# Performance work log

Hardware: AMD Instinct MI355X
Metric: run time of the kernel (lower is better)

The kernel has to match this reference:

```python
import jax, jax.numpy as jnp
import numpy as np
import math

DIM = 512      # vMF embedding dim
B = 512        # batch
K = 10         # sample_size
C = 8192       # num_classes
L = 0.7        # kappa_confidence
T_REJ = 32     # fixed rejection-sampling tries (acceptance ~0.7 per try)


def _vmf_logc(k, dim=DIM):
    # Approximate log normalizer from the paper (approximate_logc=True path).
    nm14 = (dim - 1) / 4.0
    nm12 = (dim - 1) / 2.0
    np12 = (dim + 1) / 2.0
    sqrtm = jnp.sqrt(nm12 * nm12 + k * k)
    sqrtp = jnp.sqrt(np12 * np12 + k * k)
    return nm14 * (jnp.log(nm12 + sqrtm) + jnp.log(nm12 + sqrtp)) - 0.5 * (sqrtm + sqrtp)


def _split(params):
    # params layout: [log_probs(1), means(DIM), hidden_ik(1)] (single component).
    means = params[..., 1:1 + DIM]
    hidden_ik = params[..., -1]
    mu = means / jnp.linalg.norm(means, axis=-1, keepdims=True)
    kappa = 1.0 / jnp.exp(hidden_ik)  # positive(x) = exp(x) parametrization
    return mu, kappa


def _vmf_sample(key, mu, kappa, n):
    # Wood's algorithm, vectorized over (b, n) with fixed-count rejection.
    b, d = mu.shape
    kap = kappa[:, None]  # (b,1)
    bb = (-2.0 * kap + jnp.sqrt(4.0 * kap * kap + (d - 1) ** 2)) / (d - 1)
    x0 = (1.0 - bb) / (1.0 + bb)
    cc = kap * x0 + (d - 1) * jnp.log(1.0 - x0 * x0)
    kz, ku, kv = jax.random.split(key, 3)
    z = jax.random.beta(kz, (d - 1) / 2.0, (d - 1) / 2.0, (T_REJ, b, n))
    w = (1.0 - (1.0 + bb) * z) / (1.0 - (1.0 - bb) * z)  # (T,b,n)
    u = jax.random.uniform(ku, (T_REJ, b, n), minval=1e-10)
    acc = kap * w + (d - 1) * jnp.log(1.0 - x0 * w) - cc >= jnp.log(u)
    idx = jnp.argmax(acc, axis=0)  # first accepted try
    w_sel = jnp.take_along_axis(w, idx[None], axis=0)[0]  # (b,n)
    v = jax.random.normal(kv, (b, n, d))
    v = v - jnp.einsum('bnd,bd->bn', v, mu)[..., None] * mu[:, None, :]
    v = v / jnp.linalg.norm(v, axis=-1, keepdims=True)
    sin_t = jnp.sqrt(jnp.clip(1.0 - w_sel * w_sel, 0.0))
    return w_sel[..., None] * mu[:, None, :] + sin_t[..., None] * v  # (b,n,d)


def setup_inputs() -> dict:
    key = jax.random.key(0)
    kp, kw, kl = jax.random.split(key, 3)
    # Input distribution parameters: random means, hidden_ik ~ log(1/kappa) with realistic kappa.
    parameters = jax.random.normal(kp, (B, DIM + 2), dtype=jnp.float32)
    kappa0 = L / (1.0 - L * L) * (DIM - 1) / math.sqrt(DIM)  # ~31
    parameters = parameters.at[:, -1].set(0.1 * parameters[:, -1] - math.log(kappa0))
    # Class weight, built exactly as in __init__ (non-deterministic target).
    means = jax.random.normal(kw, (C, DIM), dtype=jnp.float32) * (L / (1.0 - L * L) * (DIM - 1) / math.sqrt(DIM))
    norm = jnp.linalg.norm(means, axis=-1, keepdims=True)
    hidden_ik = jnp.log(1.0 / norm)  # ipositive = log
    weight = jnp.concatenate([jnp.zeros((C, 1), jnp.float32), means, hidden_ik], axis=-1)
    log_scale = jnp.asarray(2.773, dtype=jnp.float32)
    labels = jax.random.randint(kl, (B,), 0, C)
    return {"parameters": parameters, "weight": weight, "log_scale": log_scale, "labels": labels}


def reference(parameters, weight, log_scale, labels):
    scale = jnp.exp(log_scale)
    mu_x, kappa_x = _split(parameters)   # (b,d), (b,)
    mu_w, kappa_w = _split(weight)       # (c,d), (c,)
    sample = _vmf_sample(jax.random.key(42), mu_x, kappa_x, K)  # (b,K,d)
    sample = sample / jnp.linalg.norm(sample, axis=-1, keepdims=True)
    # logmls(b,k,c): samples have concentration k1=scale; since all means are unit,
    # ||k1*m1 + k2*m2|| = sqrt(k1^2 + k2^2 + 2*k1*k2*cos) -> single GEMM over d.
    cos = jnp.einsum('bkd,cd->bkc', sample, mu_w)
    k1 = scale
    k2 = kappa_w
    kk = jnp.sqrt(k1 * k1 + k2 * k2 + 2.0 * k1 * (k2 * cos))  # (b,K,c)
    logmls = _vmf_logc(k1) + _vmf_logc(k2)[None, None, :] - _vmf_logc(kk)
    neg_logden = jax.scipy.special.logsumexp(logmls, axis=2) - _vmf_logc(scale)  # (b,K)
    neg_lognum = scale * jnp.einsum('bd,bd->b', mu_x, mu_w[labels])
    losses = neg_logden.mean(axis=1) - neg_lognum  # (b,)
    b = parameters.shape[0]
    logits = jnp.zeros((b, C), parameters.dtype).at[jnp.arange(b), labels].set(-losses)
    return logits
```

## Files before the change

kernel.cpp:

```cpp
#include <hip/hip_runtime.h>
#include <stdint.h>

#define DIMD 512
#define BATCH 512
#define KSAMP 10
#define NCLS 8192
#define TREJ 32

typedef float f32x4 __attribute__((ext_vector_type(4)));
typedef long l2 __attribute__((ext_vector_type(2)));

__device__ inline uint64_t sm64(uint64_t x) {
  x += 0x9E3779B97F4A7C15ull;
  x = (x ^ (x >> 30)) * 0xBF58476D1CE4E5B9ull;
  x = (x ^ (x >> 27)) * 0x94D049BB133111EBull;
  return x ^ (x >> 31);
}
__device__ inline float u01(uint32_t u) {
  return ((float)u + 0.5f) * 2.3283064365386963e-10f;
}
__device__ inline float normal_from(uint64_t r) {
  float u1 = u01((uint32_t)(r >> 32));
  float u2 = u01((uint32_t)r);
  return sqrtf(-2.0f * __logf(u1)) * __cosf(6.28318530718f * u2);
}
__device__ inline float gamma255(uint64_t& ctr) {
  const float dg = 255.1666667f;
  const float cg = 0.02086730f;
  for (int i = 0; i < 16; i++) {
    uint64_t r = sm64(ctr++);
    float x = normal_from(r);
    float t = fmaf(cg, x, 1.0f);
    if (t <= 0.0f) continue;
    float v3 = t * t * t;
    uint64_t r2 = sm64(ctr++);
    float u3 = u01((uint32_t)(r2 >> 32));
    if (__logf(u3) < 0.5f * x * x + dg * (1.0f - v3 + __logf(v3))) return dg * v3;
  }
  return dg;
}
__device__ inline float wave_sum(float v) {
  #pragma unroll
  for (int o = 32; o > 0; o >>= 1) v += __shfl_down(v, o, 64);
  return __shfl(v, 0, 64);
}
__device__ inline float vmf_logc(float k) {
  float k2 = k * k;
  float sm = sqrtf(65280.25f + k2);
  float sp = sqrtf(65792.25f + k2);
  return 127.75f * (__logf(255.5f + sm) + __logf(255.5f + sp)) - 0.5f * (sm + sp);
}
__device__ inline int2 pack_fp8x8(const float* v, float s) {
  int lo = 0, hi = 0;
  lo = __builtin_amdgcn_cvt_pk_fp8_f32(v[0] * s, v[1] * s, lo, false);
  lo = __builtin_amdgcn_cvt_pk_fp8_f32(v[2] * s, v[3] * s, lo, true);
  hi = __builtin_amdgcn_cvt_pk_fp8_f32(v[4] * s, v[5] * s, hi, false);
  hi = __builtin_amdgcn_cvt_pk_fp8_f32(v[6] * s, v[7] * s, hi, true);
  return make_int2(lo, hi);
}
__device__ inline int pk_off(int l) {
  return ((l >> 3) << 6) + ((l & 3) << 4) + (((l & 7) < 4) ? 0 : 8);
}
__device__ inline void sync_lds() {
  asm volatile("s_waitcnt lgkmcnt(0)\n\ts_barrier" ::: "memory");
}

__global__ __launch_bounds__(256) void prep_sample(const float* __restrict__ weight,
                                                   const float* __restrict__ params,
                                                   const float* __restrict__ lscale,
                                                   unsigned char* __restrict__ muW8,
                                                   float4* __restrict__ cparams,
                                                   float* __restrict__ rowsum,
                                                   float4* __restrict__ out4,
                                                   unsigned char* __restrict__ Sb8) {
  int blk = blockIdx.x, tid = threadIdx.x;
  int wave = tid >> 6, lane = tid & 63;
  if (blk < 2048) {
    out4[(size_t)blk * 512 + tid]       = make_float4(0.f, 0.f, 0.f, 0.f);
    out4[(size_t)blk * 512 + 256 + tid] = make_float4(0.f, 0.f, 0.f, 0.f);
    if (blk < 20) rowsum[blk * 256 + tid] = 0.0f;

    int c = blk * 4 + wave;
    const float* wr = weight + (size_t)c * (DIMD + 2) + 1;
    float v[8];
    float n2 = 0.0f;
    #pragma unroll
    for (int j = 0; j < 8; j++) { v[j] = wr[lane * 8 + j]; n2 += v[j] * v[j]; }
    n2 = wave_sum(n2);
    float inv = rsqrtf(n2) * 16.0f;
    int2 pk = pack_fp8x8(v, inv);
    *(int2*)(muW8 + (size_t)c * 512 + pk_off(lane)) = pk;

    float hik = wr[DIMD];
    float kw = __expf(-hik);
    float k1 = __expf(lscale[0]);
    float lcw = vmf_logc(kw);
    float A2 = fmaf(k1, k1, kw * kw);
    float B2 = 2.0f * k1 * kw;
    const float X0 = 0.9238795f, X1 = 0.3826834f;
    int l3 = lane & 3;
    float Xj = (l3 == 0) ? X0 : (l3 == 1) ? X1 : (l3 == 2) ? -X1 : -X0;
    float gj = lcw - vmf_logc(sqrtf(fmaf(B2, Xj, A2)));
    float g0 = __shfl(gj, 0, 64), g1 = __shfl(gj, 1, 64);
    float g2 = __shfl(gj, 2, 64), g3 = __shfl(gj, 3, 64);
    if (lane == 0) {
      float b0 = 0.25f * (g0 + g1 + g2 + g3);
      float b1 = 0.5f * (X0 * (g0 - g3) + X1 * (g1 - g2));
      float b2 = 0.5f * 0.7071068f * ((g0 + g3) - (g1 + g2));
      float b3 = 0.5f * (X1 * (g0 - g3) - X0 * (g1 - g2));
      const float L2E = 1.4426950409f;
      const float S1 = 1.0f / 256.0f;
      cparams[c] = make_float4((b0 - b2) * L2E, (b1 - 3.0f * b3) * L2E * S1,
                               (2.0f * b2) * L2E * S1 * S1,
                               (4.0f * b3) * L2E * S1 * S1 * S1);
    }
  } else {
    int row = (blk - 2048) * 4 + wave;
    int b = row / KSAMP;
    const float* pr = params + (size_t)b * (DIMD + 2) + 1;

    float mu[8];
    float n2 = 0.0f;
    #pragma unroll
    for (int j = 0; j < 8; j++) { mu[j] = pr[lane * 8 + j]; n2 += mu[j] * mu[j]; }
    n2 = wave_sum(n2);
    float invn = rsqrtf(n2);
    #pragma unroll
    for (int j = 0; j < 8; j++) mu[j] *= invn;

    float kap = __expf(-pr[DIMD]);
    float bb = (-2.0f * kap + sqrtf(fmaf(4.0f * kap, kap, 511.0f * 511.0f))) / 511.0f;
    float x0 = (1.0f - bb) / (1.0f + bb);
    float cc = kap * x0 + 511.0f * __logf(1.0f - x0 * x0);

    uint64_t ctr = (((uint64_t)(row + 1)) << 32) | ((uint64_t)lane << 8);
    float g1 = gamma255(ctr);
    float g2 = gamma255(ctr);
    float z = g1 / (g1 + g2);
    float wt = (1.0f - (1.0f + bb) * z) / (1.0f - (1.0f - bb) * z);
    uint64_t r = sm64(ctr++);
    float u = u01((uint32_t)(r >> 32));
    float lhs = kap * wt + 511.0f * __logf(1.0f - x0 * wt) - cc;
    bool acc = (lane < TREJ) && (lhs >= __logf(fmaxf(u, 1e-10f)));
    uint64_t mask = __ballot(acc);
    int sel = mask ? (__ffsll((unsigned long long)mask) - 1) : 0;
    float w = __shfl(wt, sel, 64);

    uint64_t cbase = (((uint64_t)(row + 1)) << 32) | 0x40000000ull;
    float v[8];
    #pragma unroll
    for (int j = 0; j < 8; j++) v[j] = normal_from(sm64(cbase + (uint64_t)(lane * 8 + j)));
    float d = 0.0f;
    #pragma unroll
    for (int j = 0; j < 8; j++) d += v[j] * mu[j];
    d = wave_sum(d);
    float t2 = 0.0f;
    #pragma unroll
    for (int j = 0; j < 8; j++) { v[j] -= d * mu[j]; t2 += v[j] * v[j]; }
    t2 = wave_sum(t2);
    float ivt = rsqrtf(t2);
    float st = sqrtf(fmaxf(0.0f, 1.0f - w * w)) * ivt;
    float sv[8];
    float s2 = 0.0f;
    #pragma unroll
    for (int j = 0; j < 8; j++) { sv[j] = fmaf(st, v[j], w * mu[j]); s2 += sv[j] * sv[j]; }
    s2 = wave_sum(s2);
    float is = rsqrtf(s2) * 16.0f;
    int2 pk = pack_fp8x8(sv, is);
    *(int2*)(Sb8 + (size_t)row * 512 + pk_off(lane)) = pk;
  }
}

__global__ __launch_bounds__(512, 4) void gemm_lse(const unsigned char* __restrict__ Sb8,
                                                   const unsigned char* __restrict__ Wb8,
                                                   const float4* __restrict__ cparams,
                                                   float* __restrict__ rowsum) {
  __shared__ __align__(16) unsigned char As[2][256 * 64];
  __shared__ __align__(16) unsigned char Bs[2][128 * 64];
  int tid = threadIdx.x;
  int lane = tid & 63, wave = tid >> 6;
  int tx = lane & 15, tz = lane >> 4;

  int id = blockIdx.x;
  int xcd = id & 7, lid = id >> 3;
  int c0 = (xcd * 8 + (lid & 7)) * 128;
  int r0 = (lid >> 3) * 256;

  int srow = lane >> 2;
  int slot = lane & 3;
  int kg = slot ^ ((srow >> 1) & 3);
  const unsigned char* gA[2];
  const unsigned char* gB;
  #pragma unroll
  for (int c = 0; c < 2; c++)
    gA[c] = Sb8 + (size_t)(r0 + (wave * 2 + c) * 16 + srow) * 512 + kg * 16;
  gB = Wb8 + (size_t)(c0 + wave * 16 + srow) * 512 + kg * 16;
  int ldsAo = (wave * 2) * 1024 + lane * 16;
  int ldsBo = wave * 1024 + lane * 16;

  int wm = wave >> 1, wn = wave & 1;

  f32x4 acc[4][4];
  #pragma unroll
  for (int i = 0; i < 4; i++)
    #pragma unroll
    for (int j = 0; j < 4; j++) acc[i][j] = (f32x4){0.f, 0.f, 0.f, 0.f};

  int4 ar0[2], br0[1];
  int4 ar1[2], br1[1];

#define LOADCH(CI, AR, BR)                                   \
  { AR[0] = *(const int4*)(gA[0] + (CI) * 64);               \
    AR[1] = *(const int4*)(gA[1] + (CI) * 64);               \
    BR[0] = *(const int4*)(gB + (CI) * 64); }

#define WRITELDS(P, AR, BR)                                  \
  { *(int4*)&As[P][ldsAo]        = AR[0];                    \
    *(int4*)&As[P][ldsAo + 1024] = AR[1];                    \
    *(int4*)&Bs[P][ldsBo]        = BR[0]; }

#define COMPUTE(P)                                                        \
  { l2 af[4]; l2 bf[4];                                                   \
    int sA_ = tz ^ ((tx >> 1) & 3);                                       \
    _Pragma("unroll")                                                     \
    for (int mi = 0; mi < 4; mi++)                                        \
      af[mi] = *(const l2*)&As[P][(wm * 64 + mi * 16 + tx) * 64 + sA_ * 16]; \
    _Pragma("unroll")                                                     \
    for (int ni = 0; ni < 4; ni++)                                        \
      bf[ni] = *(const l2*)&Bs[P][(wn * 64 + ni * 16 + tx) * 64 + sA_ * 16]; \
    __builtin_amdgcn_s_setprio(1);                                        \
    _Pragma("unroll")                                                     \
    for (int mi = 0; mi < 4; mi++)                                        \
      _Pragma("unroll")                                                   \
      for (int ni = 0; ni < 4; ni++)                                      \
        acc[mi][ni] = __builtin_amdgcn_mfma_f32_16x16x32_fp8_fp8(af[mi].x, bf[ni].x, acc[mi][ni], 0, 0, 0); \
    _Pragma("unroll")                                                     \
    for (int mi = 0; mi < 4; mi++)                                        \
      _Pragma("unroll")                                                   \
      for (int ni = 0; ni < 4; ni++)                                      \
        acc[mi][ni] = __builtin_amdgcn_mfma_f32_16x16x32_fp8_fp8(af[mi].y, bf[ni].y, acc[mi][ni], 0, 0, 0); \
    __builtin_amdgcn_s_setprio(0);                                        \
  }

  LOADCH(0, ar0, br0);
  LOADCH(1, ar1, br1);
  WRITELDS(0, ar0, br0);
  sync_lds();

#define GITER_EVEN(IT)                                       \
  { if ((IT) + 2 < 8) LOADCH((IT) + 2, ar0, br0);            \
    COMPUTE(0);                                              \
    if ((IT) + 1 < 8) WRITELDS(1, ar1, br1);                 \
    if ((IT) < 7) sync_lds(); }

#define GITER_ODD(IT)                                        \
  { if ((IT) + 2 < 8) LOADCH((IT) + 2, ar1, br1);            \
    COMPUTE(1);                                              \
    if ((IT) + 1 < 8) WRITELDS(0, ar0, br0);                 \
    if ((IT) < 7) sync_lds(); }

  GITER_EVEN(0) GITER_ODD(1) GITER_EVEN(2) GITER_ODD(3)
  GITER_EVEN(4) GITER_ODD(5) GITER_EVEN(6) GITER_ODD(7)

  float4 cp[4];
  #pragma unroll
  for (int ni = 0; ni < 4; ni++) cp[ni] = cparams[c0 + wn * 64 + ni * 16 + tx];

  #pragma unroll
  for (int mi = 0; mi < 4; mi++) {
    #pragma unroll
    for (int reg = 0; reg < 4; reg++) {
      float s = 0.0f;
      #pragma unroll
      for (int ni = 0; ni < 4; ni++) {
        float cv = acc[mi][ni][reg];
        float g = fmaf(fmaf(fmaf(cp[ni].w, cv, cp[ni].z), cv, cp[ni].y), cv, cp[ni].x);
        s += exp2f(g);
      }
      #pragma unroll
      for (int o = 1; o < 16; o <<= 1) s += __shfl_xor(s, o, 64);
      if (tx == 0)
        atomicAdd(&rowsum[r0 + wm * 64 + mi * 16 + tz * 4 + reg], s);
    }
  }
}

__global__ __launch_bounds__(64) void finalize_kernel(const float* __restrict__ params,
                                                      const float* __restrict__ weight,
                                                      const float* __restrict__ rowsum,
                                                      const int* __restrict__ labels,
                                                      const float* __restrict__ lscale,
                                                      float* __restrict__ out) {
  int b = blockIdx.x;
  int lane = threadIdx.x;
  int lab = labels[b];
  const float* pr = params + (size_t)b * (DIMD + 2) + 1;
  const float* wr = weight + (size_t)lab * (DIMD + 2) + 1;
  float nx = 0.0f, nw = 0.0f, d = 0.0f;
  #pragma unroll
  for (int j = 0; j < 8; j++) {
    float xv = pr[j * 64 + lane];
    float wv = wr[j * 64 + lane];
    nx += xv * xv; nw += wv * wv; d += xv * wv;
  }
  nx = wave_sum(nx); nw = wave_sum(nw); d = wave_sum(d);
  if (lane == 0) {
    float k1 = expf(lscale[0]);
    float acc = 0.0f;
    #pragma unroll
    for (int k = 0; k < KSAMP; k++) acc += __logf(rowsum[b * KSAMP + k]);
    float loss = acc * (1.0f / KSAMP) - k1 * d * rsqrtf(nx) * rsqrtf(nw);
    out[(size_t)b * NCLS + lab] = -loss;
  }
}

extern "C" void kernel_launch(void* const* d_in, const int* in_sizes, int n_in,
                              void* d_out, int out_size, void* d_ws, size_t ws_size,
                              hipStream_t stream) {
  const float* params = (const float*)d_in[0];
  const float* weight = (const float*)d_in[1];
  const float* lscale = (const float*)d_in[2];
  const int*   labels = (const int*)d_in[3];
  float* out = (float*)d_out;
  char* ws = (char*)d_ws;

  unsigned char* muW8    = (unsigned char*)(ws);
  unsigned char* Sb8     = (unsigned char*)(ws + 4194304);
  float4*        cparams = (float4*)(ws + 6815744);
  float*         rowsum  = (float*)(ws + 6946816);

  hipLaunchKernelGGL(prep_sample, dim3(2048 + BATCH * KSAMP / 4), dim3(256), 0, stream,
                     weight, params, lscale, muW8, cparams, rowsum, (float4*)out, Sb8);
  hipLaunchKernelGGL(gemm_lse, dim3((NCLS / 128) * (BATCH * KSAMP / 256)), dim3(512), 0, stream,
                     Sb8, muW8, cparams, rowsum);
  hipLaunchKernelGGL(finalize_kernel, dim3(BATCH), dim3(64), 0, stream,
                     params, weight, rowsum, labels, lscale, out);
}
```

Baseline: 159.5 us.

## Use direct global-to-LDS loads and 256x256 tiles with phased MFMA pipeline

Rewrites the fp8 GEMM mainloop so tiles are loaded with global_load_lds straight into shared memory instead of through registers. The block tile grows from 256x128 to 256x256, with each wave computing 128x64 and launch bounds relaxed to 2 blocks per CU. The MFMA work is split into barrier-separated phases with sched barriers and priority bumps, interleaved with next-stage loads. The aim is fewer redundant loads per FLOP and better load/compute overlap. In exchange it uses more registers and LDS, and halves the grid to 640 blocks, which may leave CUs unevenly loaded.

```diff
diff --git a/kernel.cpp b/kernel.cpp
--- a/kernel.cpp
+++ b/kernel.cpp
@@ -61,8 +61,10 @@
 __device__ inline int pk_off(int l) {
   return ((l >> 3) << 6) + ((l & 3) << 4) + (((l & 7) < 4) ? 0 : 8);
 }
-__device__ inline void sync_lds() {
-  asm volatile("s_waitcnt lgkmcnt(0)\n\ts_barrier" ::: "memory");
+__device__ inline void gld16(const unsigned char* g, unsigned char* l) {
+  __builtin_amdgcn_global_load_lds(
+      (const __attribute__((address_space(1))) unsigned int*)g,
+      (__attribute__((address_space(3))) unsigned int*)l, 16, 0, 0);
 }
 
 __global__ __launch_bounds__(256) void prep_sample(const float* __restrict__ weight,
@@ -171,103 +173,119 @@
   }
 }
 
-__global__ __launch_bounds__(512, 4) void gemm_lse(const unsigned char* __restrict__ Sb8,
+__global__ __launch_bounds__(512, 2) void gemm_lse(const unsigned char* __restrict__ Sb8,
                                                    const unsigned char* __restrict__ Wb8,
                                                    const float4* __restrict__ cparams,
                                                    float* __restrict__ rowsum) {
   __shared__ __align__(16) unsigned char As[2][256 * 64];
-  __shared__ __align__(16) unsigned char Bs[2][128 * 64];
+  __shared__ __align__(16) unsigned char Bs[2][256 * 64];
   int tid = threadIdx.x;
   int lane = tid & 63, wave = tid >> 6;
   int tx = lane & 15, tz = lane >> 4;
+  int wm = wave >> 2, wn = wave & 3;
 
   int id = blockIdx.x;
   int xcd = id & 7, lid = id >> 3;
-  int c0 = (xcd * 8 + (lid & 7)) * 128;
-  int r0 = (lid >> 3) * 256;
+  int c0 = (xcd * 4 + (lid & 3)) * 256;
+  int r0 = (lid >> 2) * 256;
 
   int srow = lane >> 2;
   int slot = lane & 3;
   int kg = slot ^ ((srow >> 1) & 3);
+  int sA_ = tz ^ ((tx >> 1) & 3);
+
   const unsigned char* gA[2];
-  const unsigned char* gB;
-  #pragma unroll
-  for (int c = 0; c < 2; c++)
+  const unsigned char* gB[2];
+  #pragma unroll
+  for (int c = 0; c < 2; c++) {
     gA[c] = Sb8 + (size_t)(r0 + (wave * 2 + c) * 16 + srow) * 512 + kg * 16;
-  gB = Wb8 + (size_t)(c0 + wave * 16 + srow) * 512 + kg * 16;
-  int ldsAo = (wave * 2) * 1024 + lane * 16;
-  int ldsBo = wave * 1024 + lane * 16;
-
-  int wm = wave >> 1, wn = wave & 1;
-
-  f32x4 acc[4][4];
-  #pragma unroll
-  for (int i = 0; i < 4; i++)
+    gB[c] = Wb8 + (size_t)(c0 + (wave * 2 + c) * 16 + srow) * 512 + kg * 16;
+  }
+  int ldsX0 = (wave * 2) * 1024;
+
+  f32x4 acc[8][4];
+  #pragma unroll
+  for (int i = 0; i < 8; i++)
     #pragma unroll
     for (int j = 0; j < 4; j++) acc[i][j] = (f32x4){0.f, 0.f, 0.f, 0.f};
 
-  int4 ar0[2], br0[1];
-  int4 ar1[2], br1[1];
-
-#define LOADCH(CI, AR, BR)                                   \
-  { AR[0] = *(const int4*)(gA[0] + (CI) * 64);               \
-    AR[1] = *(const int4*)(gA[1] + (CI) * 64);               \
-    BR[0] = *(const int4*)(gB + (CI) * 64); }
-
-#define WRITELDS(P, AR, BR)                                  \
-  { *(int4*)&As[P][ldsAo]        = AR[0];                    \
-    *(int4*)&As[P][ldsAo + 1024] = AR[1];                    \
-    *(int4*)&Bs[P][ldsBo]        = BR[0]; }
-
-#define COMPUTE(P)                                                        \
-  { l2 af[4]; l2 bf[4];                                                   \
-    int sA_ = tz ^ ((tx >> 1) & 3);                                       \
-    _Pragma("unroll")                                                     \
-    for (int mi = 0; mi < 4; mi++)                                        \
-      af[mi] = *(const l2*)&As[P][(wm * 64 + mi * 16 + tx) * 64 + sA_ * 16]; \
-    _Pragma("unroll")                                                     \
-    for (int ni = 0; ni < 4; ni++)                                        \
-      bf[ni] = *(const l2*)&Bs[P][(wn * 64 + ni * 16 + tx) * 64 + sA_ * 16]; \
-    __builtin_amdgcn_s_setprio(1);                                        \
-    _Pragma("unroll")                                                     \
-    for (int mi = 0; mi < 4; mi++)                                        \
-      _Pragma("unroll")                                                   \
-      for (int ni = 0; ni < 4; ni++)                                      \
-        acc[mi][ni] = __builtin_amdgcn_mfma_f32_16x16x32_fp8_fp8(af[mi].x, bf[ni].x, acc[mi][ni], 0, 0, 0); \
-    _Pragma("unroll")                                                     \
-    for (int mi = 0; mi < 4; mi++)                                        \
-      _Pragma("unroll")                                                   \
-      for (int ni = 0; ni < 4; ni++)                                      \
-        acc[mi][ni] = __builtin_amdgcn_mfma_f32_16x16x32_fp8_fp8(af[mi].y, bf[ni].y, acc[mi][ni], 0, 0, 0); \
-    __builtin_amdgcn_s_setprio(0);                                        \
-  }
-
-  LOADCH(0, ar0, br0);
-  LOADCH(1, ar1, br1);
-  WRITELDS(0, ar0, br0);
-  sync_lds();
-
-#define GITER_EVEN(IT)                                       \
-  { if ((IT) + 2 < 8) LOADCH((IT) + 2, ar0, br0);            \
-    COMPUTE(0);                                              \
-    if ((IT) + 1 < 8) WRITELDS(1, ar1, br1);                 \
-    if ((IT) < 7) sync_lds(); }
-
-#define GITER_ODD(IT)                                        \
-  { if ((IT) + 2 < 8) LOADCH((IT) + 2, ar1, br1);            \
-    COMPUTE(1);                                              \
-    if ((IT) + 1 < 8) WRITELDS(0, ar0, br0);                 \
-    if ((IT) < 7) sync_lds(); }
-
-  GITER_EVEN(0) GITER_ODD(1) GITER_EVEN(2) GITER_ODD(3)
-  GITER_EVEN(4) GITER_ODD(5) GITER_EVEN(6) GITER_ODD(7)
+#define STAGE_A(P, CI)                                        \
+  { gld16(gA[0] + (CI) * 64, &As[P][ldsX0]);                  \
+    gld16(gA[1] + (CI) * 64, &As[P][ldsX0 + 1024]); }
+#define STAGE_B(P, CI)                                        \
+  { gld16(gB[0] + (CI) * 64, &Bs[P][ldsX0]);                  \
+    gld16(gB[1] + (CI) * 64, &Bs[P][ldsX0 + 1024]); }
+
+#define RD_A(P, MI0, AF)                                                   \
+  _Pragma("unroll")                                                        \
+  for (int mi = 0; mi < 4; mi++)                                           \
+    AF[mi] = *(const l2*)&As[P][(wm * 128 + ((MI0) + mi) * 16 + tx) * 64 + sA_ * 16];
+#define RD_B(P, BF)                                                        \
+  _Pragma("unroll")                                                        \
+  for (int ni = 0; ni < 4; ni++)                                           \
+    BF[ni] = *(const l2*)&Bs[P][(wn * 64 + ni * 16 + tx) * 64 + sA_ * 16];
+
+#define MF16(AF, BF, MIB, COMP)                                            \
+  _Pragma("unroll")                                                        \
+  for (int mi = 0; mi < 4; mi++)                                           \
+    _Pragma("unroll")                                                      \
+    for (int ni = 0; ni < 4; ni++)                                         \
+      acc[(MIB) + mi][ni] = __builtin_amdgcn_mfma_f32_16x16x32_fp8_fp8(    \
+          AF[mi].COMP, BF[ni].COMP, acc[(MIB) + mi][ni], 0, 0, 0);
+
+#define PH_IN                                                              \
+  __builtin_amdgcn_s_barrier();                                            \
+  asm volatile("s_waitcnt lgkmcnt(0)" ::: "memory");                       \
+  __builtin_amdgcn_sched_barrier(0);                                       \
+  __builtin_amdgcn_s_setprio(1);
+#define PH_OUT                                                             \
+  __builtin_amdgcn_s_setprio(0);                                           \
+  __builtin_amdgcn_sched_barrier(0);                                       \
+  __builtin_amdgcn_s_barrier();
+#define VM0 asm volatile("s_waitcnt vmcnt(0)" ::: "memory")
+
+#define GITER(T)                                                           \
+  { l2 a03[4], a47[4], bf[4];                                              \
+            \
+    RD_A(0, 0, a03) RD_B(0, bf)                                            \
+    if ((T) + 1 < 8) STAGE_A(1, (T) + 1);                                  \
+    PH_IN MF16(a03, bf, 0, x) PH_OUT                                       \
+                                             \
+    if ((T) + 1 < 8) STAGE_B(1, (T) + 1);                                  \
+    PH_IN MF16(a03, bf, 0, y) PH_OUT                                       \
+     \
+    RD_A(0, 4, a47)                                                        \
+    PH_IN MF16(a47, bf, 4, x) PH_OUT                                       \
+       \
+    VM0;                                                                   \
+    PH_IN MF16(a47, bf, 4, y) PH_OUT                                       \
+            \
+    RD_A(1, 0, a03) RD_B(1, bf)                                            \
+    if ((T) + 2 < 8) STAGE_A(0, (T) + 2);                                  \
+    PH_IN MF16(a03, bf, 0, x) PH_OUT                                       \
+                                             \
+    if ((T) + 2 < 8) STAGE_B(0, (T) + 2);                                  \
+    PH_IN MF16(a03, bf, 0, y) PH_OUT                                       \
+                                            \
+    RD_A(1, 4, a47)                                                        \
+    PH_IN MF16(a47, bf, 4, x) PH_OUT                                       \
+                                  \
+    if ((T) + 2 < 8) VM0;                                                  \
+    PH_IN MF16(a47, bf, 4, y) PH_OUT                                       \
+  }
+
+  STAGE_A(0, 0) STAGE_B(0, 0)
+  VM0;
+  __builtin_amdgcn_s_barrier();
+
+  GITER(0) GITER(2) GITER(4) GITER(6)
 
   float4 cp[4];
   #pragma unroll
   for (int ni = 0; ni < 4; ni++) cp[ni] = cparams[c0 + wn * 64 + ni * 16 + tx];
 
   #pragma unroll
-  for (int mi = 0; mi < 4; mi++) {
+  for (int mi = 0; mi < 8; mi++) {
     #pragma unroll
     for (int reg = 0; reg < 4; reg++) {
       float s = 0.0f;
@@ -280,7 +298,7 @@
       #pragma unroll
       for (int o = 1; o < 16; o <<= 1) s += __shfl_xor(s, o, 64);
       if (tx == 0)
-        atomicAdd(&rowsum[r0 + wm * 64 + mi * 16 + tz * 4 + reg], s);
+        atomicAdd(&rowsum[r0 + wm * 128 + mi * 16 + tz * 4 + reg], s);
     }
   }
 }
@@ -331,7 +349,7 @@
 
   hipLaunchKernelGGL(prep_sample, dim3(2048 + BATCH * KSAMP / 4), dim3(256), 0, stream,
                      weight, params, lscale, muW8, cparams, rowsum, (float4*)out, Sb8);
-  hipLaunchKernelGGL(gemm_lse, dim3((NCLS / 128) * (BATCH * KSAMP / 256)), dim3(512), 0, stream,
+  hipLaunchKernelGGL(gemm_lse, dim3((NCLS / 256) * (BATCH * KSAMP / 256)), dim3(512), 0, stream,
                      Sb8, muW8, cparams, rowsum);
   hipLaunchKernelGGL(finalize_kernel, dim3(BATCH), dim3(64), 0, stream,
                      params, weight, rowsum, labels, lscale, out);
```

After: 182.6 us. 1.14x slower.
